# Optimization experiments

Measured on AMD Instinct MI355X. Metric: run time of the kernel, lower is better.

## Reference

```python
import jax, jax.numpy as jnp
import numpy as np
from jax import lax


def setup_inputs() -> dict:
    key = jax.random.key(0)
    k1, k2 = jax.random.split(key)
    B, T, C, U, W = 8, 4096, 512, 512, 2
    inputs = jax.random.normal(k1, (B, T, C), dtype=jnp.float32)
    kernel = jax.random.normal(k2, (W, C, 3 * U), dtype=jnp.float32) * (1.0 / np.sqrt(W * C))
    bias = jnp.zeros((3 * U,), dtype=jnp.float32)
    return {"inputs": inputs, "kernel": kernel, "bias": bias}


def _fo_pool(x, f):
    # x, f: [B, T, U]; c_t = f_t * c_{t-1} + (1 - f_t) * x_t, c_0 = 0
    xT = jnp.swapaxes(x, 0, 1)  # [T, B, U]
    fT = jnp.swapaxes(f, 0, 1)
    c0 = jnp.zeros(x.shape[:1] + x.shape[2:], dtype=x.dtype)  # [B, U]

    def step(c, fx):
        ft, xt = fx
        c = ft * c + (1.0 - ft) * xt
        return c, c

    _, cT = lax.scan(step, c0, (fT, xT))
    return jnp.swapaxes(cT, 0, 1)  # [B, T, U]


def reference(inputs, kernel, bias):
    # Conv1D, padding='same', stride=1, NWC layout
    gates = lax.conv_general_dilated(
        inputs, kernel, window_strides=(1,), padding='SAME',
        dimension_numbers=('NWC', 'WIO', 'NWC')) + bias  # [B, T, 3U]
    x, forget, output = jnp.split(gates, 3, axis=-1)
    x = jnp.tanh(x)
    forget = jax.nn.sigmoid(forget)
    c = _fo_pool(x, forget)
    h = jax.nn.sigmoid(output) * c
    return h
```

## Files before the change

kernel.cpp:

```cpp
#include <hip/hip_runtime.h>

typedef unsigned short u16;
typedef unsigned int u32;
typedef _Float16 f16;
typedef __attribute__((ext_vector_type(8))) _Float16 half8;
typedef __attribute__((ext_vector_type(2))) __fp16 fp16x2;
typedef __attribute__((ext_vector_type(4))) float float4_;
typedef __attribute__((ext_vector_type(4))) unsigned short ushort4_;
typedef __attribute__((ext_vector_type(4))) unsigned int u32x4;

union hu { f16 h; u16 u; };

__device__ __forceinline__ u32 pkrtz(float a, float b) {
    fp16x2 t = __builtin_amdgcn_cvt_pkrtz(a, b);
    union { fp16x2 h; u32 u; } cv; cv.h = t;
    return cv.u;
}

__device__ __forceinline__ void gl16(const u16* g, u16* l) {
    __builtin_amdgcn_global_load_lds(
        (const __attribute__((address_space(1))) void*)g,
        (__attribute__((address_space(3))) void*)l, 16, 0, 0);
}

#define Bsz 8
#define Tsz 4096
#define Csz 512
#define Usz 512
#define NG  1536
#define KK  1024
#define MM  32768
#define NCH 256
#define CHL 16

__global__ void prep_a(const float* __restrict__ in, u16* __restrict__ A16) {
    int gid = blockIdx.x * 256 + threadIdx.x;
    int idx8 = gid * 8;
    int c8 = idx8 & 511;
    int row = idx8 >> 9;
    int b = (u32)row / 4097u;
    int t = row - b * 4097;
    u32x4 w;
    if (t == Tsz) {
        w = (u32x4)0;
    } else {
        const float* p = in + ((size_t)(b * Tsz + t) << 9) + c8;
        float4_ v0 = *(const float4_*)p;
        float4_ v1 = *(const float4_*)(p + 4);
        w.x = pkrtz(v0.x, v0.y); w.y = pkrtz(v0.z, v0.w);
        w.z = pkrtz(v1.x, v1.y); w.w = pkrtz(v1.z, v1.w);
    }
    *(u32x4*)(A16 + idx8) = w;
}

__global__ void prep_k(const float* __restrict__ kern, u16* __restrict__ KT) {
    __shared__ u16 t[64][70];
    const int k0 = blockIdx.x * 64;
    const int n0 = blockIdx.y * 64;
    const int tid = threadIdx.x;
    #pragma unroll
    for (int it = 0; it < 16; ++it) {
        int s = it * 256 + tid;
        int r = s >> 6;
        int c = s & 63;
        float v = kern[(size_t)(k0 + r) * NG + n0 + c];
        hu cv; cv.h = (f16)v;
        t[c][r] = cv.u;
    }
    __syncthreads();
    #pragma unroll
    for (int it = 0; it < 4; ++it) {
        int s = it * 256 + tid;
        int n = s >> 4;
        int kq = (s & 15) * 4;
        ushort4_ w;
        w.x = t[n][kq]; w.y = t[n][kq + 1]; w.z = t[n][kq + 2]; w.w = t[n][kq + 3];
        *(ushort4_*)(KT + (size_t)(n0 + n) * KK + k0 + kq) = w;
    }
}

__global__ __launch_bounds__(256, 4) void gemm_gates(
    const u16* __restrict__ A16, const u16* __restrict__ KT,
    const float* __restrict__ bias,
    u16* __restrict__ X, u16* __restrict__ F, float* __restrict__ O)
{
    __shared__ u16 lA[8192], lB[8192];

    const int tid  = threadIdx.x;
    const int lane = tid & 63;
    const int wave = tid >> 6;

    const int orig = blockIdx.x;
    const int wg = (orig & 7) * 384 + (orig >> 3);
    const int nb = wg % 12;
    const int mb = wg / 12;
    const int m0 = mb * 128;
    const int n0 = nb * 128;
    const int b  = m0 >> 12;
    const int t0 = m0 & 4095;
    const int arow0 = b * (Tsz + 1) + t0;

    float4_ acc[4][4];
    #pragma unroll
    for (int i = 0; i < 4; ++i)
        #pragma unroll
        for (int j = 0; j < 4; ++j) acc[i][j] = (float4_)0.0f;

    const int wm = (wave >> 1) * 64;
    const int wn = (wave & 1) * 64;
    const int ar = wm + (lane & 15);
    const int br = wn + (lane & 15);
    const int q  = lane >> 4;
    const int swz = lane & 7;

    for (int kc = 0; kc < KK; kc += 64) {
        __syncthreads();
        const int tap = kc >> 9;
        const int kin = kc & 511;
        const int ab = arow0 + tap;
        #pragma unroll
        for (int it = 0; it < 4; ++it) {
            const int s = it * 256 + tid;
            const int row = s >> 3, p = s & 7;
            const int c = p ^ (row & 7);
            gl16(A16 + (((size_t)(ab + row)) << 9) + kin + c * 8, lA + (s - lane) * 8);
        }
        #pragma unroll
        for (int it = 0; it < 4; ++it) {
            const int s = it * 256 + tid;
            const int row = s >> 3, p = s & 7;
            const int c = p ^ (row & 7);
            gl16(KT + (((size_t)(n0 + row)) << 10) + kc + c * 8, lB + (s - lane) * 8);
        }
        __syncthreads();

        #pragma unroll
        for (int s2 = 0; s2 < 2; ++s2) {
            half8 fa[4], fb[4];
            const int cc = (s2 * 4 + q) ^ swz;
            #pragma unroll
            for (int i = 0; i < 4; ++i) {
                fa[i] = *(const half8*)(lA + (ar + i * 16) * 64 + cc * 8);
                fb[i] = *(const half8*)(lB + (br + i * 16) * 64 + cc * 8);
            }
            #pragma unroll
            for (int mi = 0; mi < 4; ++mi)
                #pragma unroll
                for (int ni = 0; ni < 4; ++ni)
                    acc[mi][ni] = __builtin_amdgcn_mfma_f32_16x16x32_f16(fa[mi], fb[ni], acc[mi][ni], 0, 0, 0);
        }
    }

    const int plane = nb >> 2;
    const int rq = q * 4;
    const int cl = lane & 15;
    #pragma unroll
    for (int mi = 0; mi < 4; ++mi)
        #pragma unroll
        for (int ni = 0; ni < 4; ++ni) {
            const int gm = m0 + wm + mi * 16 + rq;
            const int gn = n0 + wn + ni * 16 + cl;
            const float bv = bias[gn];
            const int cp = gn & 511;
            #pragma unroll
            for (int r2 = 0; r2 < 4; ++r2) {
                float v = acc[mi][ni][r2] + bv;
                if (plane == 0) {
                    float res = 1.0f - 2.0f / (__expf(2.0f * v) + 1.0f);
                    hu cv; cv.h = (f16)res;
                    X[(size_t)(gm + r2) * Usz + cp] = cv.u;
                } else if (plane == 1) {
                    float res = 1.0f / (1.0f + __expf(-v));
                    hu cv; cv.h = (f16)res;
                    F[(size_t)(gm + r2) * Usz + cp] = cv.u;
                } else {
                    float res = 1.0f / (1.0f + __expf(-v));
                    O[(size_t)(gm + r2) * Usz + cp] = res;
                }
            }
        }
}

__device__ __forceinline__ float4_ cvt4(ushort4_ xr) {
    float4_ xv;
    #pragma unroll
    for (int j = 0; j < 4; ++j) { hu cv; cv.u = xr[j]; xv[j] = (float)cv.h; }
    return xv;
}

__global__ __launch_bounds__(256) void scan_chunk(
    const u16* __restrict__ F, const u16* __restrict__ X,
    float* __restrict__ CA, float* __restrict__ CB) {
    int g = blockIdx.x * 256 + threadIdx.x;
    int u4 = (g & 127) * 4;
    int bc = g >> 7;
    size_t base = (size_t)bc * CHL * Usz + u4;
    float4_ c = (float4_)0.0f, A = (float4_)1.0f;
    ushort4_ fcur = *(const ushort4_*)(F + base);
    ushort4_ xcur = *(const ushort4_*)(X + base);
    #pragma unroll
    for (int i = 0; i < CHL; ++i) {
        ushort4_ fnx = fcur, xnx = xcur;
        if (i + 1 < CHL) {
            fnx = *(const ushort4_*)(F + base + (size_t)(i + 1) * Usz);
            xnx = *(const ushort4_*)(X + base + (size_t)(i + 1) * Usz);
        }
        float4_ fv = cvt4(fcur);
        float4_ xv = cvt4(xcur);
        c = fv * c + (1.0f - fv) * xv;
        A = A * fv;
        fcur = fnx; xcur = xnx;
    }
    *(float4_*)(CA + (size_t)bc * Usz + u4) = A;
    *(float4_*)(CB + (size_t)bc * Usz + u4) = c;
}

__global__ __launch_bounds__(256) void scan_prefix(
    const float* __restrict__ CA, const float* __restrict__ CB,
    float* __restrict__ CS) {
    int g = blockIdx.x * 256 + threadIdx.x;
    int u = g & 511;
    int b = g >> 9;
    float c = 0.0f;
    #pragma unroll 8
    for (int ch = 0; ch < NCH; ++ch) {
        int idx = (b * NCH + ch) * Usz + u;
        CS[idx] = c;
        c = CA[idx] * c + CB[idx];
    }
}

__global__ __launch_bounds__(256) void scan_final(
    const u16* __restrict__ F, const u16* __restrict__ X,
    const float* __restrict__ CS, float* __restrict__ out) {
    int g = blockIdx.x * 256 + threadIdx.x;
    int u4 = (g & 127) * 4;
    int bc = g >> 7;
    size_t base = (size_t)bc * CHL * Usz + u4;
    float4_ c = *(const float4_*)(CS + (size_t)bc * Usz + u4);
    ushort4_ fcur = *(const ushort4_*)(F + base);
    ushort4_ xcur = *(const ushort4_*)(X + base);
    #pragma unroll
    for (int i = 0; i < CHL; ++i) {
        ushort4_ fnx = fcur, xnx = xcur;
        if (i + 1 < CHL) {
            fnx = *(const ushort4_*)(F + base + (size_t)(i + 1) * Usz);
            xnx = *(const ushort4_*)(X + base + (size_t)(i + 1) * Usz);
        }
        float4_ fv = cvt4(fcur);
        float4_ xv = cvt4(xcur);
        c = fv * c + (1.0f - fv) * xv;
        float4_ ov = *(const float4_*)(out + base + (size_t)i * Usz);
        *(float4_*)(out + base + (size_t)i * Usz) = ov * c;
        fcur = fnx; xcur = xnx;
    }
}

extern "C" void kernel_launch(void* const* d_in, const int* in_sizes, int n_in,
                              void* d_out, int out_size, void* d_ws, size_t ws_size,
                              hipStream_t stream) {
    const float* in   = (const float*)d_in[0];
    const float* kern = (const float*)d_in[1];
    const float* bias = (const float*)d_in[2];
    float* out = (float*)d_out;
    char* ws = (char*)d_ws;

    const size_t A16_B  = (size_t)Bsz * (Tsz + 1) * Csz * 2;
    const size_t OFF_KT = A16_B;
    const size_t OFF_F  = OFF_KT + (size_t)NG * KK * 2;
    const size_t OFF_X  = OFF_F + (size_t)MM * Usz * 2;
    const size_t NEED   = OFF_X + (size_t)MM * Usz * 2;

    if (ws_size < NEED) return;

    u16*   A16 = (u16*)ws;
    u16*   KT  = (u16*)(ws + OFF_KT);
    u16*   Fh  = (u16*)(ws + OFF_F);
    u16*   Xb  = (u16*)(ws + OFF_X);
    const size_t CH = (size_t)Bsz * NCH * Usz;
    float* CA = (float*)ws;
    float* CB = CA + CH;
    float* CS = CB + CH;

    prep_a<<<(int)(A16_B / 16 / 256), 256, 0, stream>>>(in, A16);
    prep_k<<<dim3(KK / 64, NG / 64), 256, 0, stream>>>(kern, KT);
    gemm_gates<<<(MM / 128) * (NG / 128), 256, 0, stream>>>(A16, KT, bias, Xb, Fh, out);
    scan_chunk<<<Bsz * NCH * Usz / 4 / 256, 256, 0, stream>>>(Fh, Xb, CA, CB);
    scan_prefix<<<Bsz * Usz / 256, 256, 0, stream>>>(CA, CB, CS);
    scan_final<<<Bsz * NCH * Usz / 4 / 256, 256, 0, stream>>>(Fh, Xb, CS, out);
}
```

Measured before the change: 302.7 us.

## Split serial chunk prefix scan into a three-level segmented scan

Replaces the single serial 256-step inter-chunk prefix kernel, which launched only 16 blocks, with three kernels. The first reduces segments of 16 chunks, the second does a 16-step prefix over the segments, and the third expands the segment prefixes back to per-chunk prefixes. This exposes 16x more threads to hide memory latency. The cost is two extra kernel launches and extra reads of CA/CB.

```diff
diff --git a/kernel.cpp b/kernel.cpp
--- a/kernel.cpp
+++ b/kernel.cpp
@@ -32,6 +32,8 @@
 #define MM  32768
 #define NCH 256
 #define CHL 16
+#define SEG 16
+#define NSEG 16
 
 __global__ void prep_a(const float* __restrict__ in, u16* __restrict__ A16) {
     int gid = blockIdx.x * 256 + threadIdx.x;
@@ -215,16 +217,53 @@
     *(float4_*)(CB + (size_t)bc * Usz + u4) = c;
 }
 
-__global__ __launch_bounds__(256) void scan_prefix(
+__global__ __launch_bounds__(256) void scan_seg(
     const float* __restrict__ CA, const float* __restrict__ CB,
-    float* __restrict__ CS) {
+    float* __restrict__ SA, float* __restrict__ SB) {
+    int g = blockIdx.x * 256 + threadIdx.x;
+    int u = g & 511;
+    int t2 = g >> 9;
+    int s = t2 & (NSEG - 1);
+    int b = t2 >> 4;
+    float A = 1.0f, Bv = 0.0f;
+    #pragma unroll
+    for (int k = 0; k < SEG; ++k) {
+        int idx = (b * NCH + s * SEG + k) * Usz + u;
+        float a = CA[idx], bb = CB[idx];
+        Bv = a * Bv + bb;
+        A  = a * A;
+    }
+    int o = (b * NSEG + s) * Usz + u;
+    SA[o] = A; SB[o] = Bv;
+}
+
+__global__ __launch_bounds__(256) void scan_segpfx(
+    const float* __restrict__ SA, const float* __restrict__ SB,
+    float* __restrict__ CSS) {
     int g = blockIdx.x * 256 + threadIdx.x;
     int u = g & 511;
     int b = g >> 9;
     float c = 0.0f;
-    #pragma unroll 8
-    for (int ch = 0; ch < NCH; ++ch) {
-        int idx = (b * NCH + ch) * Usz + u;
+    #pragma unroll
+    for (int s = 0; s < NSEG; ++s) {
+        int o = (b * NSEG + s) * Usz + u;
+        CSS[o] = c;
+        c = SA[o] * c + SB[o];
+    }
+}
+
+__global__ __launch_bounds__(256) void scan_expand(
+    const float* __restrict__ CA, const float* __restrict__ CB,
+    const float* __restrict__ CSS, float* __restrict__ CS) {
+    int g = blockIdx.x * 256 + threadIdx.x;
+    int u = g & 511;
+    int t2 = g >> 9;
+    int s = t2 & (NSEG - 1);
+    int b = t2 >> 4;
+    float c = CSS[(b * NSEG + s) * Usz + u];
+    #pragma unroll
+    for (int k = 0; k < SEG; ++k) {
+        int idx = (b * NCH + s * SEG + k) * Usz + u;
         CS[idx] = c;
         c = CA[idx] * c + CB[idx];
     }
@@ -277,15 +316,21 @@
     u16*   KT  = (u16*)(ws + OFF_KT);
     u16*   Fh  = (u16*)(ws + OFF_F);
     u16*   Xb  = (u16*)(ws + OFF_X);
-    const size_t CH = (size_t)Bsz * NCH * Usz;
-    float* CA = (float*)ws;
-    float* CB = CA + CH;
-    float* CS = CB + CH;
+    const size_t CH  = (size_t)Bsz * NCH * Usz;
+    const size_t CHS = (size_t)Bsz * NSEG * Usz;
+    float* CA  = (float*)ws;
+    float* CB  = CA + CH;
+    float* CS  = CB + CH;
+    float* SA  = CS + CH;
+    float* SB  = SA + CHS;
+    float* CSS = SB + CHS;
 
     prep_a<<<(int)(A16_B / 16 / 256), 256, 0, stream>>>(in, A16);
     prep_k<<<dim3(KK / 64, NG / 64), 256, 0, stream>>>(kern, KT);
     gemm_gates<<<(MM / 128) * (NG / 128), 256, 0, stream>>>(A16, KT, bias, Xb, Fh, out);
     scan_chunk<<<Bsz * NCH * Usz / 4 / 256, 256, 0, stream>>>(Fh, Xb, CA, CB);
-    scan_prefix<<<Bsz * Usz / 256, 256, 0, stream>>>(CA, CB, CS);
+    scan_seg<<<Bsz * NSEG * Usz / 256, 256, 0, stream>>>(CA, CB, SA, SB);
+    scan_segpfx<<<Bsz * Usz / 256, 256, 0, stream>>>(SA, SB, CSS);
+    scan_expand<<<Bsz * NSEG * Usz / 256, 256, 0, stream>>>(CA, CB, CSS, CS);
     scan_final<<<Bsz * NCH * Usz / 4 / 256, 256, 0, stream>>>(Fh, Xb, CS, out);
 }
```

After: 290.3 us. 1.04x faster.
